# Kernel optimization log

Hardware: AMD Instinct MI355X
Metric: run time of the kernel (lower is better)

Reference implementation:

```python
import jax, jax.numpy as jnp
import numpy as np

N = 100000   # nodes
E = 1600000  # edges (avg degree 16)
IN, H, OUT, P = 100, 256, 256, 128
EPS = 1e-5


def setup_inputs() -> dict:
    key = jax.random.key(0)
    ks = jax.random.split(key, 12)

    def lin(k, o, i):
        return jax.random.normal(k, (o, i), jnp.float32) / np.float32(np.sqrt(i))

    return {
        "x": jax.random.normal(ks[0], (N, IN), jnp.float32),
        "edge_index": jax.random.randint(ks[1], (2, E), 0, N),
        # SAGEConv l (aggregated-neighbor branch, has bias) and r (root branch, no bias)
        "Wl0": lin(ks[2], H, IN), "bl0": jnp.zeros((H,), jnp.float32), "Wr0": lin(ks[3], H, IN),
        "Wl1": lin(ks[4], H, H),  "bl1": jnp.zeros((H,), jnp.float32), "Wr1": lin(ks[5], H, H),
        "Wl2": lin(ks[6], OUT, H), "bl2": jnp.zeros((OUT,), jnp.float32), "Wr2": lin(ks[7], OUT, H),
        # projection head + BatchNorm1d(128)
        "Wp": lin(ks[8], P, OUT), "bp": jnp.zeros((P,), jnp.float32),
        "gamma": jnp.ones((P,), jnp.float32), "beta": jnp.zeros((P,), jnp.float32),
    }


def _sage_conv(x, src, dst, Wl, bl, Wr):
    # PyG SAGEConv default: mean-aggregate source features into destinations,
    # then lin_l(agg) + lin_r(x).
    agg = jax.ops.segment_sum(x[src], dst, num_segments=N)           # [N, d]
    deg = jax.ops.segment_sum(jnp.ones((src.shape[0],), x.dtype), dst, num_segments=N)
    agg = agg / jnp.maximum(deg, 1.0)[:, None]
    return agg @ Wl.T + bl + x @ Wr.T


def reference(x, edge_index, Wl0, bl0, Wr0, Wl1, bl1, Wr1, Wl2, bl2, Wr2, Wp, bp, gamma, beta):
    src, dst = edge_index[0], edge_index[1]
    x = jax.nn.relu(_sage_conv(x, src, dst, Wl0, bl0, Wr0))  # dropout is identity in eval
    x = jax.nn.relu(_sage_conv(x, src, dst, Wl1, bl1, Wr1))
    x = _sage_conv(x, src, dst, Wl2, bl2, Wr2)               # no relu on last layer
    z = x @ Wp.T + bp                                        # projection head -> [N, 128]
    mu = jnp.mean(z, axis=0)
    var = jnp.var(z, axis=0)                                 # biased, as torch BN uses for normalization
    h = gamma * (z - mu) * jax.lax.rsqrt(var + EPS) + beta
    return (x, h)
```

## Files before the change

### kernel.cpp

```cpp
#include <hip/hip_runtime.h>
#include <hip/hip_bf16.h>

#define EPS_BN 1e-5f

using short8  = __attribute__((ext_vector_type(8))) short;
using ushort8 = __attribute__((ext_vector_type(8))) unsigned short;
using f32x4   = __attribute__((ext_vector_type(4))) float;

typedef const __attribute__((address_space(1))) void* gas_ptr;
typedef __attribute__((address_space(3))) void* las_ptr;

__device__ inline float bf2f(unsigned short u) {
    union { unsigned i; float f; } c; c.i = ((unsigned)u) << 16; return c.f;
}
__device__ inline unsigned short f2bf(float f) {
    unsigned x = __float_as_uint(f);
    unsigned r = (x + 0x7FFF + ((x >> 16) & 1)) >> 16;
    return (unsigned short)r;
}

__global__ void zero_i32(int* __restrict__ p, int n) {
    int i = blockIdx.x * blockDim.x + threadIdx.x;
    if (i < n) p[i] = 0;
}
__global__ void zero_f32(float* __restrict__ p, int n) {
    int i = blockIdx.x * blockDim.x + threadIdx.x;
    if (i < n) p[i] = 0.0f;
}

__global__ void conv_w(const float* __restrict__ w, unsigned short* __restrict__ o,
                       int R, int C, int CP) {
    int t = blockIdx.x * blockDim.x + threadIdx.x;
    if (t >= R * CP) return;
    int r = t / CP, c = t % CP;
    o[t] = (c < C) ? f2bf(w[(size_t)r * C + c]) : (unsigned short)0;
}

__global__ void conv_x_pad(const float* __restrict__ x, unsigned short* __restrict__ xp, int n) {
    int t = blockIdx.x * blockDim.x + threadIdx.x;
    if (t >= n * 32) return;
    int node = t >> 5, g = t & 31;
    int f0 = g * 4;
    ushort4 o;
    const float* xr = x + (size_t)node * 100;
    o.x = (f0 + 0 < 100) ? f2bf(xr[f0 + 0]) : 0;
    o.y = (f0 + 1 < 100) ? f2bf(xr[f0 + 1]) : 0;
    o.z = (f0 + 2 < 100) ? f2bf(xr[f0 + 2]) : 0;
    o.w = (f0 + 3 < 100) ? f2bf(xr[f0 + 3]) : 0;
    *(ushort4*)(xp + (size_t)node * 128 + f0) = o;
}

__global__ void count_k(const int* __restrict__ dst, int* __restrict__ counts, int E) {
    int i = blockIdx.x * blockDim.x + threadIdx.x;
    if (i < E) atomicAdd(&counts[dst[i]], 1);
}

__global__ void scan1(const int* __restrict__ counts, int* __restrict__ rp,
                      int* __restrict__ partials, int n) {
    __shared__ int s[256];
    int t = threadIdx.x;
    int i = blockIdx.x * 256 + t;
    int v = (i < n) ? counts[i] : 0;
    s[t] = v;
    __syncthreads();
    for (int off = 1; off < 256; off <<= 1) {
        int u = (t >= off) ? s[t - off] : 0;
        __syncthreads();
        s[t] += u;
        __syncthreads();
    }
    if (i < n) rp[i] = s[t] - v;
    if (t == 255) partials[blockIdx.x] = s[255];
}

__global__ void scan2(int* __restrict__ partials, int nb) {
    __shared__ int s[512];
    int t = threadIdx.x;
    int v = (t < nb) ? partials[t] : 0;
    s[t] = v;
    __syncthreads();
    for (int off = 1; off < 512; off <<= 1) {
        int u = (t >= off) ? s[t - off] : 0;
        __syncthreads();
        s[t] += u;
        __syncthreads();
    }
    if (t < nb) partials[t] = s[t] - v;
}

__global__ void scan3(int* __restrict__ rp, const int* __restrict__ partials, int n, int E) {
    int i = blockIdx.x * blockDim.x + threadIdx.x;
    if (i < n) rp[i] += partials[i >> 8];
    if (i == 0) rp[n] = E;
}

__global__ void fill_k(const int* __restrict__ src, const int* __restrict__ dst,
                       const int* __restrict__ rp, int* __restrict__ cursor,
                       int* __restrict__ col, int E) {
    int i = blockIdx.x * blockDim.x + threadIdx.x;
    if (i < E) {
        int d = dst[i];
        int pos = atomicAdd(&cursor[d], 1);
        col[rp[d] + pos] = src[i];
    }
}

__global__ __launch_bounds__(256) void agg_bf16_256(
    const unsigned short* __restrict__ x, const int* __restrict__ rp,
    const int* __restrict__ col, unsigned short* __restrict__ out, int n) {
    int wave = threadIdx.x >> 6, lane = threadIdx.x & 63;
    int node = blockIdx.x * 4 + wave;
    if (node >= n) return;
    int s = rp[node], e = rp[node + 1];
    int deg = e - s;
    int h = lane >> 5;
    int l32 = lane & 31;

    float a[8] = {0, 0, 0, 0, 0, 0, 0, 0};
    int base = 0;
    for (; base + 8 <= deg; base += 8) {
        int i = s + base + h;
        int r0 = col[i], r1 = col[i + 2], r2 = col[i + 4], r3 = col[i + 6];
        ushort8 v0 = *(const ushort8*)(x + (size_t)r0 * 256 + l32 * 8);
        ushort8 v1 = *(const ushort8*)(x + (size_t)r1 * 256 + l32 * 8);
        ushort8 v2 = *(const ushort8*)(x + (size_t)r2 * 256 + l32 * 8);
        ushort8 v3 = *(const ushort8*)(x + (size_t)r3 * 256 + l32 * 8);
#pragma unroll
        for (int j = 0; j < 8; ++j)
            a[j] += bf2f(v0[j]) + bf2f(v1[j]) + bf2f(v2[j]) + bf2f(v3[j]);
    }
    for (int i = s + base + h; i < e; i += 2) {
        int r = col[i];
        ushort8 v = *(const ushort8*)(x + (size_t)r * 256 + l32 * 8);
#pragma unroll
        for (int j = 0; j < 8; ++j) a[j] += bf2f(v[j]);
    }
#pragma unroll
    for (int j = 0; j < 8; ++j) a[j] += __shfl_xor(a[j], 32);

    if (h == 0) {
        float sc = 1.0f / fmaxf((float)deg, 1.0f);
        ushort8 o;
#pragma unroll
        for (int j = 0; j < 8; ++j) o[j] = f2bf(a[j] * sc);
        *(ushort8*)(out + (size_t)node * 256 + l32 * 8) = o;
    }
}

__global__ __launch_bounds__(256) void agg_bf16_128(
    const unsigned short* __restrict__ x, const int* __restrict__ rp,
    const int* __restrict__ col, unsigned short* __restrict__ out, int n) {
    int wave = threadIdx.x >> 6, lane = threadIdx.x & 63;
    int node = blockIdx.x * 4 + wave;
    if (node >= n) return;
    int s = rp[node], e = rp[node + 1];
    int deg = e - s;
    int q = lane >> 4;
    int l16 = lane & 15;

    float a[8] = {0, 0, 0, 0, 0, 0, 0, 0};
    int base = 0;
    for (; base + 16 <= deg; base += 16) {
        int i = s + base + q;
        int r0 = col[i], r1 = col[i + 4], r2 = col[i + 8], r3 = col[i + 12];
        ushort8 v0 = *(const ushort8*)(x + (size_t)r0 * 128 + l16 * 8);
        ushort8 v1 = *(const ushort8*)(x + (size_t)r1 * 128 + l16 * 8);
        ushort8 v2 = *(const ushort8*)(x + (size_t)r2 * 128 + l16 * 8);
        ushort8 v3 = *(const ushort8*)(x + (size_t)r3 * 128 + l16 * 8);
#pragma unroll
        for (int j = 0; j < 8; ++j)
            a[j] += bf2f(v0[j]) + bf2f(v1[j]) + bf2f(v2[j]) + bf2f(v3[j]);
    }
    for (int i = s + base + q; i < e; i += 4) {
        int r = col[i];
        ushort8 v = *(const ushort8*)(x + (size_t)r * 128 + l16 * 8);
#pragma unroll
        for (int j = 0; j < 8; ++j) a[j] += bf2f(v[j]);
    }
#pragma unroll
    for (int j = 0; j < 8; ++j) {
        a[j] += __shfl_xor(a[j], 16);
        a[j] += __shfl_xor(a[j], 32);
    }

    if (lane < 16) {
        float sc = 1.0f / fmaxf((float)deg, 1.0f);
        ushort8 o;
#pragma unroll
        for (int j = 0; j < 8; ++j) o[j] = f2bf(a[j] * sc);
        *(ushort8*)(out + (size_t)node * 128 + l16 * 8) = o;
    }
}

template <int KTOT, int DOUT, bool HAS_AGG, bool RELU, bool STF32, bool STBF16>
__global__ __launch_bounds__(512) void sage_mfma(
    const unsigned short* __restrict__ xp, const unsigned short* __restrict__ ap,
    const unsigned short* __restrict__ Wr, const unsigned short* __restrict__ Wl,
    const float* __restrict__ bias,
    float* __restrict__ outf, unsigned short* __restrict__ outb, int n) {
    constexpr int CT = DOUT / 16;
    constexpr int NSRC = HAS_AGG ? 2 : 1;
    constexpr int FR = NSRC == 2 ? DOUT * 4 : DOUT * 4;
    constexpr int CHUNKS = NSRC * CT;
    constexpr int CPW = CHUNKS / 8;
    constexpr int KS = KTOT / 32;
    constexpr int BUFSZ = NSRC * FR * 8;
    __shared__ __align__(16) unsigned short lds[2 * BUFSZ];

    const int t = threadIdx.x;
    const int wave = t >> 6, lane = t & 63;
    const int node0 = blockIdx.x * 128 + wave * 16;
    const bool active = node0 < n;
    const int lcol = lane & 15, lq = lane >> 4;

    auto stage = [&](int ks, int buf) {
        unsigned short* base = lds + buf * BUFSZ;
#pragma unroll
        for (int i = 0; i < CPW; ++i) {
            int chunk = wave * CPW + i;
            int srcSel = chunk / CT, ct = chunk % CT;
            const unsigned short* W = (srcSel == 0) ? Wr : Wl;
            const unsigned short* g = W + (size_t)(ct * 16 + lcol) * KTOT + ks * 32 + lq * 8;
            unsigned short* l = base + chunk * 512;
            __builtin_amdgcn_global_load_lds((gas_ptr)g, (las_ptr)l, 16, 0, 0);
        }
    };

    f32x4 acc[CT];
#pragma unroll
    for (int c = 0; c < CT; ++c) {
        float b = bias[c * 16 + lcol];
        acc[c][0] = b; acc[c][1] = b; acc[c][2] = b; acc[c][3] = b;
    }

    const unsigned short* aRow  = xp + (size_t)(node0 + lcol) * KTOT + lq * 8;
    const unsigned short* aRow2 = HAS_AGG ? (ap + (size_t)(node0 + lcol) * KTOT + lq * 8) : xp;

    stage(0, 0);
    __syncthreads();

    for (int ks = 0; ks < KS; ++ks) {
        if (ks + 1 < KS) stage(ks + 1, (ks + 1) & 1);
        if (active) {
            short8 a = *(const short8*)(aRow + ks * 32);
            const short8* bf = (const short8*)(lds + (ks & 1) * BUFSZ);
#pragma unroll
            for (int c = 0; c < CT; ++c)
                acc[c] = __builtin_amdgcn_mfma_f32_16x16x32_bf16(a, bf[c * 64 + lane], acc[c], 0, 0, 0);
            if (HAS_AGG) {
                short8 a2 = *(const short8*)(aRow2 + ks * 32);
                const short8* bf2 = bf + FR;
#pragma unroll
                for (int c = 0; c < CT; ++c)
                    acc[c] = __builtin_amdgcn_mfma_f32_16x16x32_bf16(a2, bf2[c * 64 + lane], acc[c], 0, 0, 0);
            }
        }
        __syncthreads();
    }
    if (!active) return;

#pragma unroll
    for (int c = 0; c < CT; ++c) {
        f32x4 v = acc[c];
        if (RELU) {
            v[0] = fmaxf(v[0], 0.0f); v[1] = fmaxf(v[1], 0.0f);
            v[2] = fmaxf(v[2], 0.0f); v[3] = fmaxf(v[3], 0.0f);
        }
#pragma unroll
        for (int j = 0; j < 4; ++j) {
            size_t row = (size_t)node0 + lq * 4 + j;
            int colI = c * 16 + lcol;
            if (STF32) outf[row * DOUT + colI] = v[j];
            if (STBF16) outb[row * DOUT + colI] = f2bf(v[j]);
        }
    }
}

__global__ void bn_partial(const float* __restrict__ z, float* __restrict__ sums, int n) {
    int f = threadIdx.x & 127;
    int half = threadIdx.x >> 7;
    float s = 0.0f, s2 = 0.0f;
    for (int row = blockIdx.x * 2 + half; row < n; row += gridDim.x * 2) {
        float v = z[(size_t)row * 128 + f];
        s += v; s2 += v * v;
    }
    __shared__ float ls[256], ls2[256];
    ls[threadIdx.x] = s; ls2[threadIdx.x] = s2;
    __syncthreads();
    if (half == 0) {
        atomicAdd(&sums[f], s + ls[128 + f]);
        atomicAdd(&sums[128 + f], s2 + ls2[128 + f]);
    }
}

__global__ void bn_finalize(const float* __restrict__ sums, const float* __restrict__ gamma,
                            const float* __restrict__ beta, float* __restrict__ params, int n) {
    int f = threadIdx.x;
    float mu = sums[f] / (float)n;
    float var = sums[128 + f] / (float)n - mu * mu;
    float inv = rsqrtf(var + EPS_BN);
    float sc = gamma[f] * inv;
    params[f] = sc;
    params[128 + f] = beta[f] - mu * sc;
}

__global__ void bn_apply(float* __restrict__ z, const float* __restrict__ params, int total4) {
    int i = blockIdx.x * blockDim.x + threadIdx.x;
    for (; i < total4; i += gridDim.x * blockDim.x) {
        float4 v = ((float4*)z)[i];
        int f0 = (i & 31) * 4;
        v.x = v.x * params[f0 + 0] + params[128 + f0 + 0];
        v.y = v.y * params[f0 + 1] + params[128 + f0 + 1];
        v.z = v.z * params[f0 + 2] + params[128 + f0 + 2];
        v.w = v.w * params[f0 + 3] + params[128 + f0 + 3];
        ((float4*)z)[i] = v;
    }
}

extern "C" void kernel_launch(void* const* d_in, const int* in_sizes, int n_in,
                              void* d_out, int out_size, void* d_ws, size_t ws_size,
                              hipStream_t stream) {
    const float* x_in  = (const float*)d_in[0];
    const int*   ei    = (const int*)d_in[1];
    const float* Wl0   = (const float*)d_in[2];
    const float* bl0   = (const float*)d_in[3];
    const float* Wr0   = (const float*)d_in[4];
    const float* Wl1   = (const float*)d_in[5];
    const float* bl1   = (const float*)d_in[6];
    const float* Wr1   = (const float*)d_in[7];
    const float* Wl2   = (const float*)d_in[8];
    const float* bl2   = (const float*)d_in[9];
    const float* Wr2   = (const float*)d_in[10];
    const float* Wp    = (const float*)d_in[11];
    const float* bp    = (const float*)d_in[12];
    const float* gamma = (const float*)d_in[13];
    const float* beta  = (const float*)d_in[14];

    const int IN = 100, INP = 128, H = 256, OUT = 256, P = 128;
    const int n = in_sizes[0] / IN;
    const int E = in_sizes[1] / 2;
    const int* src = ei;
    const int* dst = ei + E;

    size_t off = 0;
    auto alloc = [&](size_t bytes) -> char* {
        char* p = (char*)d_ws + off;
        off += (bytes + 255) & ~(size_t)255;
        return p;
    };
    int*   counts   = (int*)alloc((size_t)n * 4);
    int*   cursor   = (int*)alloc((size_t)n * 4);
    int*   rp       = (int*)alloc((size_t)(n + 1) * 4);
    int*   partials = (int*)alloc(512 * 4);
    int*   col      = (int*)alloc((size_t)E * 4);
    unsigned short* Wl0b = (unsigned short*)alloc((size_t)H * INP * 2);
    unsigned short* Wr0b = (unsigned short*)alloc((size_t)H * INP * 2);
    unsigned short* Wl1b = (unsigned short*)alloc((size_t)H * H * 2);
    unsigned short* Wr1b = (unsigned short*)alloc((size_t)H * H * 2);
    unsigned short* Wl2b = (unsigned short*)alloc((size_t)OUT * H * 2);
    unsigned short* Wr2b = (unsigned short*)alloc((size_t)OUT * H * 2);
    unsigned short* Wpb  = (unsigned short*)alloc((size_t)P * OUT * 2);
    float* bnsums   = (float*)alloc(256 * 4);
    float* bnparams = (float*)alloc(256 * 4);
    unsigned short* bufA = (unsigned short*)alloc((size_t)n * H * 2);
    unsigned short* bufB = (unsigned short*)alloc((size_t)n * H * 2);
    unsigned short* bufC = (unsigned short*)alloc((size_t)n * H * 2);
    unsigned short* bufD = (unsigned short*)alloc((size_t)n * H * 2);

    unsigned short* xpad   = bufA;
    unsigned short* aggpad = bufA + (size_t)n * INP;
    unsigned short* h1b  = bufB;
    unsigned short* agg1 = bufC;
    unsigned short* h2b  = bufD;
    unsigned short* agg2 = bufB;
    unsigned short* xb2  = bufA;

    float* out_x = (float*)d_out;
    float* z     = out_x + (size_t)n * OUT;

    const int nb = (n + 255) / 256;
    const int gemm_grid = (n + 127) / 128;

    zero_i32<<<nb, 256, 0, stream>>>(counts, n);
    zero_i32<<<nb, 256, 0, stream>>>(cursor, n);
    zero_f32<<<1, 256, 0, stream>>>(bnsums, 256);
    count_k<<<(E + 255) / 256, 256, 0, stream>>>(dst, counts, E);
    scan1<<<nb, 256, 0, stream>>>(counts, rp, partials, n);
    scan2<<<1, 512, 0, stream>>>(partials, nb);
    scan3<<<nb, 256, 0, stream>>>(rp, partials, n, E);
    fill_k<<<(E + 255) / 256, 256, 0, stream>>>(src, dst, rp, cursor, col, E);

    conv_x_pad<<<(n * 32 + 255) / 256, 256, 0, stream>>>(x_in, xpad, n);
    conv_w<<<(H * INP + 255) / 256, 256, 0, stream>>>(Wl0, Wl0b, H, IN, INP);
    conv_w<<<(H * INP + 255) / 256, 256, 0, stream>>>(Wr0, Wr0b, H, IN, INP);
    conv_w<<<(H * H + 255) / 256, 256, 0, stream>>>(Wl1, Wl1b, H, H, H);
    conv_w<<<(H * H + 255) / 256, 256, 0, stream>>>(Wr1, Wr1b, H, H, H);
    conv_w<<<(OUT * H + 255) / 256, 256, 0, stream>>>(Wl2, Wl2b, OUT, H, H);
    conv_w<<<(OUT * H + 255) / 256, 256, 0, stream>>>(Wr2, Wr2b, OUT, H, H);
    conv_w<<<(P * OUT + 255) / 256, 256, 0, stream>>>(Wp, Wpb, P, OUT, OUT);

    agg_bf16_128<<<(n + 3) / 4, 256, 0, stream>>>(xpad, rp, col, aggpad, n);
    sage_mfma<128, 256, true, true, false, true><<<gemm_grid, 512, 0, stream>>>(
        xpad, aggpad, Wr0b, Wl0b, bl0, nullptr, h1b, n);

    agg_bf16_256<<<(n + 3) / 4, 256, 0, stream>>>(h1b, rp, col, agg1, n);
    sage_mfma<256, 256, true, true, false, true><<<gemm_grid, 512, 0, stream>>>(
        h1b, agg1, Wr1b, Wl1b, bl1, nullptr, h2b, n);

    agg_bf16_256<<<(n + 3) / 4, 256, 0, stream>>>(h2b, rp, col, agg2, n);
    sage_mfma<256, 256, true, false, true, true><<<gemm_grid, 512, 0, stream>>>(
        h2b, agg2, Wr2b, Wl2b, bl2, out_x, xb2, n);

    sage_mfma<256, 128, false, false, true, false><<<gemm_grid, 512, 0, stream>>>(
        xb2, nullptr, Wpb, nullptr, bp, z, nullptr, n);

    bn_partial<<<256, 256, 0, stream>>>(z, bnsums, n);
    bn_finalize<<<1, 128, 0, stream>>>(bnsums, gamma, beta, bnparams, n);
    bn_apply<<<2048, 256, 0, stream>>>(z, bnparams, n * (P / 4));
}
```

Before: 742.4 us.

## Pad CSR rows to multiples of eight with zero-row sentinel to remove tail loops

Row lengths in the CSR are rounded up to multiples of eight, and a pad_fill kernel fills the extra slots with an index pointing at an appended all-zero feature row. The aggregation kernels then run only full unrolled batches with no scalar remainder loop, and the 256-wide version loads eight neighbors per iteration for more memory-level parallelism. The cost is extra padded gathers (about 3.5 per node on average), a larger col array, separate feature buffers with an extra row each, and two small extra kernels.

```diff
diff --git a/kernel.cpp b/kernel.cpp
--- a/kernel.cpp
+++ b/kernel.cpp
@@ -26,6 +26,15 @@
 __global__ void zero_f32(float* __restrict__ p, int n) {
     int i = blockIdx.x * blockDim.x + threadIdx.x;
     if (i < n) p[i] = 0.0f;
+}
+
+__global__ void zero_rows(unsigned short* __restrict__ xpad,
+                          unsigned short* __restrict__ h1,
+                          unsigned short* __restrict__ h2, int n) {
+    int t = threadIdx.x;
+    if (t < 128) xpad[(size_t)n * 128 + t] = 0;
+    h1[(size_t)n * 256 + t] = 0;
+    h2[(size_t)n * 256 + t] = 0;
 }
 
 __global__ void conv_w(const float* __restrict__ w, unsigned short* __restrict__ o,
@@ -60,7 +69,7 @@
     __shared__ int s[256];
     int t = threadIdx.x;
     int i = blockIdx.x * 256 + t;
-    int v = (i < n) ? counts[i] : 0;
+    int v = (i < n) ? ((counts[i] + 7) & ~7) : 0;
     s[t] = v;
     __syncthreads();
     for (int off = 1; off < 256; off <<= 1) {
@@ -88,10 +97,9 @@
     if (t < nb) partials[t] = s[t] - v;
 }
 
-__global__ void scan3(int* __restrict__ rp, const int* __restrict__ partials, int n, int E) {
+__global__ void scan3(int* __restrict__ rp, const int* __restrict__ partials, int n) {
     int i = blockIdx.x * blockDim.x + threadIdx.x;
     if (i < n) rp[i] += partials[i >> 8];
-    if (i == 0) rp[n] = E;
 }
 
 __global__ void fill_k(const int* __restrict__ src, const int* __restrict__ dst,
@@ -105,35 +113,58 @@
     }
 }
 
+__global__ void pad_fill(const int* __restrict__ rp, const int* __restrict__ cnt,
+                         int* __restrict__ col, int n, int zrow) {
+    int node = blockIdx.x * blockDim.x + threadIdx.x;
+    if (node >= n) return;
+    int d = cnt[node];
+    int s = rp[node] + d;
+    int e = rp[node] + ((d + 7) & ~7);
+    for (int i = s; i < e; ++i) col[i] = zrow;
+}
+
 __global__ __launch_bounds__(256) void agg_bf16_256(
     const unsigned short* __restrict__ x, const int* __restrict__ rp,
-    const int* __restrict__ col, unsigned short* __restrict__ out, int n) {
+    const int* __restrict__ cnt, const int* __restrict__ col,
+    unsigned short* __restrict__ out, int n) {
     int wave = threadIdx.x >> 6, lane = threadIdx.x & 63;
     int node = blockIdx.x * 4 + wave;
     if (node >= n) return;
-    int s = rp[node], e = rp[node + 1];
-    int deg = e - s;
+    int s = rp[node];
+    int deg = cnt[node];
+    int nb8 = (deg + 7) >> 3;
     int h = lane >> 5;
     int l32 = lane & 31;
+    const size_t coff = (size_t)l32 * 8;
 
     float a[8] = {0, 0, 0, 0, 0, 0, 0, 0};
-    int base = 0;
-    for (; base + 8 <= deg; base += 8) {
-        int i = s + base + h;
+    int i = s + h;
+    int b = 0;
+    for (; b + 2 <= nb8; b += 2, i += 16) {
+        int r0 = col[i],     r1 = col[i + 2],  r2 = col[i + 4],  r3 = col[i + 6];
+        int r4 = col[i + 8], r5 = col[i + 10], r6 = col[i + 12], r7 = col[i + 14];
+        ushort8 v0 = *(const ushort8*)(x + (size_t)r0 * 256 + coff);
+        ushort8 v1 = *(const ushort8*)(x + (size_t)r1 * 256 + coff);
+        ushort8 v2 = *(const ushort8*)(x + (size_t)r2 * 256 + coff);
+        ushort8 v3 = *(const ushort8*)(x + (size_t)r3 * 256 + coff);
+        ushort8 v4 = *(const ushort8*)(x + (size_t)r4 * 256 + coff);
+        ushort8 v5 = *(const ushort8*)(x + (size_t)r5 * 256 + coff);
+        ushort8 v6 = *(const ushort8*)(x + (size_t)r6 * 256 + coff);
+        ushort8 v7 = *(const ushort8*)(x + (size_t)r7 * 256 + coff);
+#pragma unroll
+        for (int j = 0; j < 8; ++j)
+            a[j] += ((bf2f(v0[j]) + bf2f(v1[j])) + (bf2f(v2[j]) + bf2f(v3[j]))) +
+                    ((bf2f(v4[j]) + bf2f(v5[j])) + (bf2f(v6[j]) + bf2f(v7[j])));
+    }
+    if (b < nb8) {
         int r0 = col[i], r1 = col[i + 2], r2 = col[i + 4], r3 = col[i + 6];
-        ushort8 v0 = *(const ushort8*)(x + (size_t)r0 * 256 + l32 * 8);
-        ushort8 v1 = *(const ushort8*)(x + (size_t)r1 * 256 + l32 * 8);
-        ushort8 v2 = *(const ushort8*)(x + (size_t)r2 * 256 + l32 * 8);
-        ushort8 v3 = *(const ushort8*)(x + (size_t)r3 * 256 + l32 * 8);
+        ushort8 v0 = *(const ushort8*)(x + (size_t)r0 * 256 + coff);
+        ushort8 v1 = *(const ushort8*)(x + (size_t)r1 * 256 + coff);
+        ushort8 v2 = *(const ushort8*)(x + (size_t)r2 * 256 + coff);
+        ushort8 v3 = *(const ushort8*)(x + (size_t)r3 * 256 + coff);
 #pragma unroll
         for (int j = 0; j < 8; ++j)
-            a[j] += bf2f(v0[j]) + bf2f(v1[j]) + bf2f(v2[j]) + bf2f(v3[j]);
-    }
-    for (int i = s + base + h; i < e; i += 2) {
-        int r = col[i];
-        ushort8 v = *(const ushort8*)(x + (size_t)r * 256 + l32 * 8);
-#pragma unroll
-        for (int j = 0; j < 8; ++j) a[j] += bf2f(v[j]);
+            a[j] += (bf2f(v0[j]) + bf2f(v1[j])) + (bf2f(v2[j]) + bf2f(v3[j]));
     }
 #pragma unroll
     for (int j = 0; j < 8; ++j) a[j] += __shfl_xor(a[j], 32);
@@ -149,33 +180,37 @@
 
 __global__ __launch_bounds__(256) void agg_bf16_128(
     const unsigned short* __restrict__ x, const int* __restrict__ rp,
-    const int* __restrict__ col, unsigned short* __restrict__ out, int n) {
+    const int* __restrict__ cnt, const int* __restrict__ col,
+    unsigned short* __restrict__ out, int n) {
     int wave = threadIdx.x >> 6, lane = threadIdx.x & 63;
     int node = blockIdx.x * 4 + wave;
     if (node >= n) return;
-    int s = rp[node], e = rp[node + 1];
-    int deg = e - s;
+    int s = rp[node];
+    int deg = cnt[node];
+    int nb8 = (deg + 7) >> 3;
     int q = lane >> 4;
     int l16 = lane & 15;
+    const size_t coff = (size_t)l16 * 8;
 
     float a[8] = {0, 0, 0, 0, 0, 0, 0, 0};
-    int base = 0;
-    for (; base + 16 <= deg; base += 16) {
-        int i = s + base + q;
+    int i = s + q;
+    int b = 0;
+    for (; b + 2 <= nb8; b += 2, i += 16) {
         int r0 = col[i], r1 = col[i + 4], r2 = col[i + 8], r3 = col[i + 12];
-        ushort8 v0 = *(const ushort8*)(x + (size_t)r0 * 128 + l16 * 8);
-        ushort8 v1 = *(const ushort8*)(x + (size_t)r1 * 128 + l16 * 8);
-        ushort8 v2 = *(const ushort8*)(x + (size_t)r2 * 128 + l16 * 8);
-        ushort8 v3 = *(const ushort8*)(x + (size_t)r3 * 128 + l16 * 8);
+        ushort8 v0 = *(const ushort8*)(x + (size_t)r0 * 128 + coff);
+        ushort8 v1 = *(const ushort8*)(x + (size_t)r1 * 128 + coff);
+        ushort8 v2 = *(const ushort8*)(x + (size_t)r2 * 128 + coff);
+        ushort8 v3 = *(const ushort8*)(x + (size_t)r3 * 128 + coff);
 #pragma unroll
         for (int j = 0; j < 8; ++j)
-            a[j] += bf2f(v0[j]) + bf2f(v1[j]) + bf2f(v2[j]) + bf2f(v3[j]);
-    }
-    for (int i = s + base + q; i < e; i += 4) {
-        int r = col[i];
-        ushort8 v = *(const ushort8*)(x + (size_t)r * 128 + l16 * 8);
-#pragma unroll
-        for (int j = 0; j < 8; ++j) a[j] += bf2f(v[j]);
+            a[j] += (bf2f(v0[j]) + bf2f(v1[j])) + (bf2f(v2[j]) + bf2f(v3[j]));
+    }
+    if (b < nb8) {
+        int r0 = col[i], r1 = col[i + 4];
+        ushort8 v0 = *(const ushort8*)(x + (size_t)r0 * 128 + coff);
+        ushort8 v1 = *(const ushort8*)(x + (size_t)r1 * 128 + coff);
+#pragma unroll
+        for (int j = 0; j < 8; ++j) a[j] += bf2f(v0[j]) + bf2f(v1[j]);
     }
 #pragma unroll
     for (int j = 0; j < 8; ++j) {
@@ -200,7 +235,7 @@
     float* __restrict__ outf, unsigned short* __restrict__ outb, int n) {
     constexpr int CT = DOUT / 16;
     constexpr int NSRC = HAS_AGG ? 2 : 1;
-    constexpr int FR = NSRC == 2 ? DOUT * 4 : DOUT * 4;
+    constexpr int FR = DOUT * 4;
     constexpr int CHUNKS = NSRC * CT;
     constexpr int CPW = CHUNKS / 8;
     constexpr int KS = KTOT / 32;
@@ -352,7 +387,7 @@
     int*   cursor   = (int*)alloc((size_t)n * 4);
     int*   rp       = (int*)alloc((size_t)(n + 1) * 4);
     int*   partials = (int*)alloc(512 * 4);
-    int*   col      = (int*)alloc((size_t)E * 4);
+    int*   col      = (int*)alloc(((size_t)E + 8 * (size_t)n) * 4);
     unsigned short* Wl0b = (unsigned short*)alloc((size_t)H * INP * 2);
     unsigned short* Wr0b = (unsigned short*)alloc((size_t)H * INP * 2);
     unsigned short* Wl1b = (unsigned short*)alloc((size_t)H * H * 2);
@@ -362,24 +397,20 @@
     unsigned short* Wpb  = (unsigned short*)alloc((size_t)P * OUT * 2);
     float* bnsums   = (float*)alloc(256 * 4);
     float* bnparams = (float*)alloc(256 * 4);
-    unsigned short* bufA = (unsigned short*)alloc((size_t)n * H * 2);
-    unsigned short* bufB = (unsigned short*)alloc((size_t)n * H * 2);
-    unsigned short* bufC = (unsigned short*)alloc((size_t)n * H * 2);
-    unsigned short* bufD = (unsigned short*)alloc((size_t)n * H * 2);
-
-    unsigned short* xpad   = bufA;
-    unsigned short* aggpad = bufA + (size_t)n * INP;
-    unsigned short* h1b  = bufB;
-    unsigned short* agg1 = bufC;
-    unsigned short* h2b  = bufD;
-    unsigned short* agg2 = bufB;
-    unsigned short* xb2  = bufA;
+    unsigned short* xpad   = (unsigned short*)alloc((size_t)(n + 1) * INP * 2);
+    unsigned short* aggpad = (unsigned short*)alloc((size_t)n * INP * 2);
+    unsigned short* h1b    = (unsigned short*)alloc((size_t)(n + 1) * H * 2);
+    unsigned short* agg1   = (unsigned short*)alloc((size_t)n * H * 2);
+    unsigned short* h2b    = (unsigned short*)alloc((size_t)(n + 1) * H * 2);
+    (void)alloc((size_t)256 * 512);
+
+    unsigned short* agg2 = h1b;
+    unsigned short* xb2  = xpad;
 
     float* out_x = (float*)d_out;
     float* z     = out_x + (size_t)n * OUT;
 
     const int nb = (n + 255) / 256;
-    const int gemm_grid = (n + 127) / 128;
 
     zero_i32<<<nb, 256, 0, stream>>>(counts, n);
     zero_i32<<<nb, 256, 0, stream>>>(cursor, n);
@@ -387,10 +418,12 @@
     count_k<<<(E + 255) / 256, 256, 0, stream>>>(dst, counts, E);
     scan1<<<nb, 256, 0, stream>>>(counts, rp, partials, n);
     scan2<<<1, 512, 0, stream>>>(partials, nb);
-    scan3<<<nb, 256, 0, stream>>>(rp, partials, n, E);
+    scan3<<<nb, 256, 0, stream>>>(rp, partials, n);
     fill_k<<<(E + 255) / 256, 256, 0, stream>>>(src, dst, rp, cursor, col, E);
+    pad_fill<<<nb, 256, 0, stream>>>(rp, counts, col, n, n);
 
     conv_x_pad<<<(n * 32 + 255) / 256, 256, 0, stream>>>(x_in, xpad, n);
+    zero_rows<<<1, 256, 0, stream>>>(xpad, h1b, h2b, n);
     conv_w<<<(H * INP + 255) / 256, 256, 0, stream>>>(Wl0, Wl0b, H, IN, INP);
     conv_w<<<(H * INP + 255) / 256, 256, 0, stream>>>(Wr0, Wr0b, H, IN, INP);
     conv_w<<<(H * H + 255) / 256, 256, 0, stream>>>(Wl1, Wl1b, H, H, H);
@@ -399,15 +432,17 @@
     conv_w<<<(OUT * H + 255) / 256, 256, 0, stream>>>(Wr2, Wr2b, OUT, H, H);
     conv_w<<<(P * OUT + 255) / 256, 256, 0, stream>>>(Wp, Wpb, P, OUT, OUT);
 
-    agg_bf16_128<<<(n + 3) / 4, 256, 0, stream>>>(xpad, rp, col, aggpad, n);
+    const int gemm_grid = (n + 127) / 128;
+
+    agg_bf16_128<<<(n + 3) / 4, 256, 0, stream>>>(xpad, rp, counts, col, aggpad, n);
     sage_mfma<128, 256, true, true, false, true><<<gemm_grid, 512, 0, stream>>>(
         xpad, aggpad, Wr0b, Wl0b, bl0, nullptr, h1b, n);
 
-    agg_bf16_256<<<(n + 3) / 4, 256, 0, stream>>>(h1b, rp, col, agg1, n);
+    agg_bf16_256<<<(n + 3) / 4, 256, 0, stream>>>(h1b, rp, counts, col, agg1, n);
     sage_mfma<256, 256, true, true, false, true><<<gemm_grid, 512, 0, stream>>>(
         h1b, agg1, Wr1b, Wl1b, bl1, nullptr, h2b, n);
 
-    agg_bf16_256<<<(n + 3) / 4, 256, 0, stream>>>(h2b, rp, col, agg2, n);
+    agg_bf16_256<<<(n + 3) / 4, 256, 0, stream>>>(h2b, rp, counts, col, agg2, n);
     sage_mfma<256, 256, true, false, true, true><<<gemm_grid, 512, 0, stream>>>(
         h2b, agg2, Wr2b, Wl2b, bl2, out_x, xb2, n);
 
```

Measured after the change: 746.6 us. No clear change (+0.6%).
